# Optimization experiments

Hardware: AMD Instinct MI355X
Metric: run time of the kernel (lower is better)

## Reference

```python
import jax, jax.numpy as jnp
import numpy as np

N_NODES = 50000
N_EDGES = 800000
IN_CH = 64
OC = 16  # out_channels


def setup_inputs() -> dict:
    key = jax.random.key(0)
    ks = jax.random.split(key, 16)
    x = jax.random.normal(ks[0], (N_NODES, IN_CH), dtype=jnp.float32)
    edge_index = jax.random.randint(ks[1], (2, N_EDGES), 0, N_NODES, dtype=jnp.int64)

    def lin(k, fan_in, fan_out):
        s = 1.0 / np.sqrt(fan_in)
        return jax.random.uniform(k, (fan_in, fan_out), jnp.float32, -s, s)

    d1, d2 = 16 * OC, 8 * OC  # 256, 128
    return {
        "x": x,
        "W1_rel": lin(ks[2], IN_CH, d1), "b1": jnp.zeros((d1,), jnp.float32), "W1_root": lin(ks[3], IN_CH, d1),
        "W2_rel": lin(ks[4], d1, d2), "b2": jnp.zeros((d2,), jnp.float32), "W2_root": lin(ks[5], d1, d2),
        "Wmu_rel": lin(ks[6], d2, OC), "bmu": jnp.zeros((OC,), jnp.float32), "Wmu_root": lin(ks[7], d2, OC),
        "Wls_rel": lin(ks[8], d2, OC), "bls": jnp.zeros((OC,), jnp.float32), "Wls_root": lin(ks[9], d2, OC),
        "edge_index": edge_index,
    }


def _graph_conv(x, src, dst, deg_inv, W_rel, b, W_root):
    # PyG GraphConv(aggr='mean'): out = lin_rel(mean_{j in N(i)} x_j) + lin_root(x_i)
    msg_sum = jax.ops.segment_sum(x[src], dst, num_segments=x.shape[0])  # [N, d]
    agg = msg_sum * deg_inv[:, None]
    return agg @ W_rel + b + x @ W_root


def reference(x, W1_rel, b1, W1_root, W2_rel, b2, W2_root,
              Wmu_rel, bmu, Wmu_root, Wls_rel, bls, Wls_root, edge_index):
    src, dst = edge_index[0], edge_index[1]
    deg = jax.ops.segment_sum(jnp.ones_like(dst, dtype=x.dtype), dst, num_segments=x.shape[0])
    deg_inv = jnp.where(deg > 0, 1.0 / jnp.maximum(deg, 1.0), 0.0)

    h = jax.nn.relu(_graph_conv(x, src, dst, deg_inv, W1_rel, b1, W1_root))
    h = jax.nn.relu(_graph_conv(h, src, dst, deg_inv, W2_rel, b2, W2_root))
    mu = _graph_conv(h, src, dst, deg_inv, Wmu_rel, bmu, Wmu_root)
    logstd = _graph_conv(h, src, dst, deg_inv, Wls_rel, bls, Wls_root)
    return (mu, logstd)
```

## Files before the change

### kernel.cpp

```cpp
#include <hip/hip_runtime.h>
#include <hip/hip_fp8.h>

#define N_NODES 50000
#define N_EDGES 800000
#define NBUCK 196
#define PBLK 391
#define CAP 5120

typedef unsigned short ushort_t;
typedef unsigned char uchar_t;
typedef short short8 __attribute__((ext_vector_type(8)));
typedef short short4v __attribute__((ext_vector_type(4)));
typedef float floatx4 __attribute__((ext_vector_type(4)));
typedef float floatx2 __attribute__((ext_vector_type(2)));

__device__ __forceinline__ float bf2f(ushort_t u) {
    unsigned v = ((unsigned)u) << 16;
    return __builtin_bit_cast(float, v);
}
__device__ __forceinline__ ushort_t f2bf(float f) {
    unsigned u = __builtin_bit_cast(unsigned, f);
    unsigned r = (u + 0x7FFFu + ((u >> 16) & 1u)) >> 16;
    return (ushort_t)r;
}
__device__ __forceinline__ uchar_t f2fp8(float f) {
    return (uchar_t)(__builtin_amdgcn_cvt_pk_fp8_f32(f, f, 0, false) & 0xFF);
}
__device__ __forceinline__ float4 ld4(const float* p) { return *(const float4*)p; }

__device__ __forceinline__ void lite_barrier() {
    asm volatile("s_waitcnt lgkmcnt(0)" ::: "memory");
    __builtin_amdgcn_s_barrier();
}

__device__ __forceinline__ void acc16(float* a, uint4 v) {
    unsigned ws[4] = {v.x, v.y, v.z, v.w};
    #pragma unroll
    for (int wi = 0; wi < 4; ++wi) {
        floatx2 lo = __builtin_amdgcn_cvt_pk_f32_fp8(ws[wi], false);
        floatx2 hi = __builtin_amdgcn_cvt_pk_f32_fp8(ws[wi], true);
        a[wi * 4 + 0] += lo.x; a[wi * 4 + 1] += lo.y;
        a[wi * 4 + 2] += hi.x; a[wi * 4 + 3] += hi.y;
    }
}
__device__ __forceinline__ void acc8(float* a, uint2 v) {
    floatx2 p0 = __builtin_amdgcn_cvt_pk_f32_fp8(v.x, false);
    floatx2 p1 = __builtin_amdgcn_cvt_pk_f32_fp8(v.x, true);
    floatx2 p2 = __builtin_amdgcn_cvt_pk_f32_fp8(v.y, false);
    floatx2 p3 = __builtin_amdgcn_cvt_pk_f32_fp8(v.y, true);
    a[0] += p0.x; a[1] += p0.y; a[2] += p1.x; a[3] += p1.y;
    a[4] += p2.x; a[5] += p2.y; a[6] += p3.x; a[7] += p3.y;
}

__global__ __launch_bounds__(256) void prep_kernel(
    const float* __restrict__ x,
    const float* __restrict__ W1_rel, const float* __restrict__ W1_root,
    const float* __restrict__ W2_rel, const float* __restrict__ W2_root,
    const float* __restrict__ Wmu_rel, const float* __restrict__ Wls_rel,
    const float* __restrict__ Wmu_root, const float* __restrict__ Wls_root,
    ushort_t* __restrict__ xb, uchar_t* __restrict__ xq,
    ushort_t* __restrict__ B1t, ushort_t* __restrict__ B2t, ushort_t* __restrict__ B3t,
    int* __restrict__ bcursor) {
    int idx = blockIdx.x * blockDim.x + threadIdx.x;
    if (idx < 400000) {
        int n = idx >> 3, c = (idx & 7) * 8;
        float4 v0 = ld4(x + (size_t)n * 64 + c);
        float4 v1 = ld4(x + (size_t)n * 64 + c + 4);
        float vv[8] = {v0.x, v0.y, v0.z, v0.w, v1.x, v1.y, v1.z, v1.w};
        short8 o;
        #pragma unroll
        for (int i = 0; i < 8; ++i) o[i] = f2bf(vv[i]);
        int q0 = __builtin_amdgcn_cvt_pk_fp8_f32(vv[0], vv[1], 0, false);
        q0 = __builtin_amdgcn_cvt_pk_fp8_f32(vv[2], vv[3], q0, true);
        int q1 = __builtin_amdgcn_cvt_pk_fp8_f32(vv[4], vv[5], 0, false);
        q1 = __builtin_amdgcn_cvt_pk_fp8_f32(vv[6], vv[7], q1, true);
        *(short8*)(xb + (size_t)n * 64 + c) = o;
        uint2 q = {(unsigned)q0, (unsigned)q1};
        *(uint2*)(xq + (size_t)n * 64 + c) = q;
    } else if (idx < 506496) {
        int j = idx - 400000;
        if (j < 32768) {
            int n = j >> 7, k = j & 127;
            float v = (k < 64) ? W1_rel[k * 256 + n] : W1_root[(k - 64) * 256 + n];
            B1t[j] = f2bf(v);
        } else if (j < 98304) {
            int jj = j - 32768;
            int n = jj >> 8, k = jj & 255;
            float v = (n < 128) ? W2_rel[k * 128 + n] : W2_root[k * 128 + (n - 128)];
            B2t[jj] = f2bf(v);
        } else {
            int jj = j - 98304;
            int n = jj >> 7, k = jj & 127;
            const float* W = (n < 16) ? Wmu_rel : (n < 32) ? Wls_rel : (n < 48) ? Wmu_root : Wls_root;
            B3t[jj] = f2bf(W[k * 16 + (n & 15)]);
        }
    } else if (idx < 506496 + NBUCK) {
        int b = idx - 506496;
        bcursor[b] = b * CAP;
    }
}

__global__ __launch_bounds__(512) void partition_kernel(
    const int* __restrict__ src, const int* __restrict__ dst,
    int* __restrict__ bcursor, unsigned* __restrict__ pairbuf) {
    __shared__ int h[NBUCK];
    __shared__ int cur[NBUCK];
    const int tid = threadIdx.x;
    for (int i = tid; i < NBUCK; i += 512) h[i] = 0;
    __syncthreads();
    const int base = blockIdx.x * 2048;
    int d[4];
    #pragma unroll
    for (int j = 0; j < 4; ++j) {
        int e = base + j * 512 + tid;
        if (e < N_EDGES) { d[j] = dst[e]; atomicAdd(&h[d[j] >> 8], 1); }
        else d[j] = -1;
    }
    __syncthreads();
    for (int i = tid; i < NBUCK; i += 512) {
        int c = h[i];
        cur[i] = c ? atomicAdd(&bcursor[i], c) : 0;
    }
    __syncthreads();
    #pragma unroll
    for (int j = 0; j < 4; ++j) {
        int e = base + j * 512 + tid;
        if (e < N_EDGES) {
            int dd = d[j];
            int slot = atomicAdd(&cur[dd >> 8], 1);
            pairbuf[slot] = (unsigned)src[e] | ((unsigned)(dd & 255) << 16);
        }
    }
}

__global__ __launch_bounds__(1024) void fill_bucket_kernel(
    const unsigned* __restrict__ pairbuf, const int* __restrict__ bcursor,
    int* __restrict__ row_beg, int* __restrict__ row_end,
    float* __restrict__ dinv, ushort_t* __restrict__ eidx) {
    __shared__ int h[256];
    __shared__ int sm[256];
    __shared__ int cur[256];
    const int b = blockIdx.x, tid = threadIdx.x;
    const int beg = b * CAP, end = bcursor[b];
    if (tid < 256) h[tid] = 0;
    __syncthreads();
    for (int i = beg + tid; i < end; i += 1024)
        atomicAdd(&h[pairbuf[i] >> 16], 1);
    __syncthreads();
    if (tid < 256) sm[tid] = h[tid];
    __syncthreads();
    #pragma unroll
    for (int off = 1; off < 256; off <<= 1) {
        int t = 0;
        if (tid < 256 && tid >= off) t = sm[tid - off];
        __syncthreads();
        if (tid < 256) sm[tid] += t;
        __syncthreads();
    }
    if (tid < 256) {
        int c = h[tid];
        int exc = beg + sm[tid] - c;
        int node = b * 256 + tid;
        if (node < N_NODES) {
            row_beg[node] = exc;
            row_end[node] = exc + c;
            dinv[node] = c > 0 ? 1.0f / (float)c : 0.0f;
        }
        cur[tid] = exc;
    }
    __syncthreads();
    for (int i = beg + tid; i < end; i += 1024) {
        unsigned v = pairbuf[i];
        int slot = atomicAdd(&cur[v >> 16], 1);
        eidx[slot] = (ushort_t)(v & 0xFFFFu);
    }
}

__global__ __launch_bounds__(256) void g1gemm12(
    const ushort_t* __restrict__ xb, const uchar_t* __restrict__ xq,
    const int* __restrict__ row_beg, const int* __restrict__ row_end,
    const ushort_t* __restrict__ eidx, const float* __restrict__ dinv,
    const ushort_t* __restrict__ B1t, const float* __restrict__ b1,
    const ushort_t* __restrict__ B2t, ushort_t* __restrict__ h1g,
    uchar_t* __restrict__ t2, ushort_t* __restrict__ r2) {
    constexpr int K1 = 128, K2 = 256;
    constexpr int AKP = 72;
    constexpr int BKP = 136;
    __shared__ ushort_t Bs[64 * BKP];
    ushort_t* As = Bs;
    const int tid = threadIdx.x;
    const int rowbase = blockIdx.x * 64;

    {
        const int nl = tid >> 2, lane = tid & 3;
        const int node = rowbase + nl;
        int beg = 0, end = 0;
        float d = 0.0f;
        if (node < N_NODES) { beg = row_beg[node]; end = row_end[node]; d = dinv[node]; }
        float a0[16] = {}, a1[16] = {};
        int j = beg;
        for (; j + 3 < end; j += 4) {
            uint4 v0 = *(const uint4*)(xq + (size_t)eidx[j] * 64 + lane * 16);
            uint4 v1 = *(const uint4*)(xq + (size_t)eidx[j + 1] * 64 + lane * 16);
            uint4 v2 = *(const uint4*)(xq + (size_t)eidx[j + 2] * 64 + lane * 16);
            uint4 v3 = *(const uint4*)(xq + (size_t)eidx[j + 3] * 64 + lane * 16);
            acc16(a0, v0); acc16(a1, v1); acc16(a0, v2); acc16(a1, v3);
        }
        for (; j < end; ++j) {
            uint4 v0 = *(const uint4*)(xq + (size_t)eidx[j] * 64 + lane * 16);
            acc16(a0, v0);
        }
        short8 o0, o1;
        #pragma unroll
        for (int i = 0; i < 8; ++i) {
            o0[i] = f2bf((a0[i] + a1[i]) * d);
            o1[i] = f2bf((a0[8 + i] + a1[8 + i]) * d);
        }
        *(short8*)(As + nl * AKP + lane * 16) = o0;
        *(short8*)(As + nl * AKP + lane * 16 + 8) = o1;
    }
    __syncthreads();

    const int w = tid >> 6, lane64 = tid & 63;
    const int ln = lane64 & 15, quad = lane64 >> 4;
    const int rwl = w * 16 + ln;
    int r = rowbase + rwl;
    if (r > N_NODES - 1) r = N_NODES - 1;

    float bias[4][4];
    #pragma unroll
    for (int ny = 0; ny < 4; ++ny)
        #pragma unroll
        for (int f = 0; f < 4; ++f)
            bias[ny][f] = b1[ny * 64 + f * 16 + ln];

    short8 a[4];
    a[0] = *(const short8*)(As + rwl * AKP + quad * 8);
    a[1] = *(const short8*)(As + rwl * AKP + 32 + quad * 8);
    a[2] = *(const short8*)(xb + (size_t)r * 64 + quad * 8);
    a[3] = *(const short8*)(xb + (size_t)r * 64 + 32 + quad * 8);
    short8 pb[4];
    #pragma unroll
    for (int i = 0; i < 4; ++i) {
        int idx = tid + i * 256, row = idx >> 4, off = (idx & 15) * 8;
        pb[i] = *(const short8*)(B1t + (size_t)row * K1 + off);
    }
    for (int ny = 0; ny < 4; ++ny) {
        lite_barrier();
        #pragma unroll
        for (int i = 0; i < 4; ++i) {
            int idx = tid + i * 256, row = idx >> 4, off = (idx & 15) * 8;
            *(short8*)(Bs + row * BKP + off) = pb[i];
        }
        if (ny < 3) {
            #pragma unroll
            for (int i = 0; i < 4; ++i) {
                int idx = tid + i * 256, row = idx >> 4, off = (idx & 15) * 8;
                pb[i] = *(const short8*)(B1t + (size_t)((ny + 1) * 64 + row) * K1 + off);
            }
        } else {
            #pragma unroll
            for (int i = 0; i < 4; ++i) {
                int idx = tid + i * 256, row = idx >> 4, off = (idx & 15) * 8;
                pb[i] = *(const short8*)(B2t + (size_t)row * K2 + off);
            }
        }
        lite_barrier();
        floatx4 acc[4] = {};
        #pragma unroll
        for (int f = 0; f < 4; ++f) {
            const ushort_t* bp = Bs + (f * 16 + ln) * BKP + quad * 8;
            #pragma unroll
            for (int s = 0; s < 4; ++s) {
                short8 b = *(const short8*)(bp + s * 32);
                acc[f] = __builtin_amdgcn_mfma_f32_16x16x32_bf16(a[s], b, acc[f], 0, 0, 0);
            }
        }
        lite_barrier();
        #pragma unroll
        for (int f = 0; f < 4; ++f) {
            int nl0 = f * 16 + ln;
            #pragma unroll
            for (int g = 0; g < 4; ++g) {
                int rr = w * 16 + quad * 4 + g;
                Bs[rr * AKP + nl0] = f2bf(fmaxf(acc[f][g] + bias[ny][f], 0.0f));
            }
        }
        lite_barrier();
        {
            int row2 = tid >> 2, seg = tid & 3;
            int gr = rowbase + row2;
            if (gr < N_NODES) {
                const uint4* s4 = (const uint4*)(Bs + row2 * AKP + seg * 16);
                uint4* d4 = (uint4*)(h1g + (size_t)gr * 256 + ny * 64 + seg * 16);
                d4[0] = s4[0]; d4[1] = s4[1];
            }
        }
    }
    __syncthreads();

    short8 a2[8];
    #pragma unroll
    for (int s = 0; s < 8; ++s)
        a2[s] = *(const short8*)(h1g + (size_t)r * 256 + s * 32 + quad * 8);
    for (int ny = 0; ny < 4; ++ny) {
        floatx4 acc[4] = {};
        #pragma unroll
        for (int kh = 0; kh < 2; ++kh) {
            lite_barrier();
            #pragma unroll
            for (int i = 0; i < 4; ++i) {
                int idx = tid + i * 256, row = idx >> 4, off = (idx & 15) * 8;
                *(short8*)(Bs + row * BKP + off) = pb[i];
            }
            int st = ny * 2 + kh;
            if (st < 7) {
                int nyn = (st + 1) >> 1, khn = (st + 1) & 1;
                #pragma unroll
                for (int i = 0; i < 4; ++i) {
                    int idx = tid + i * 256, row = idx >> 4, off = (idx & 15) * 8;
                    pb[i] = *(const short8*)(B2t + (size_t)(nyn * 64 + row) * K2 + khn * 128 + off);
                }
            }
            lite_barrier();
            #pragma unroll
            for (int f = 0; f < 4; ++f) {
                const ushort_t* bp = Bs + (f * 16 + ln) * BKP + quad * 8;
                #pragma unroll
                for (int s = 0; s < 4; ++s) {
                    short8 b = *(const short8*)(bp + s * 32);
                    acc[f] = __builtin_amdgcn_mfma_f32_16x16x32_bf16(a2[kh * 4 + s], b, acc[f], 0, 0, 0);
                }
            }
        }
        lite_barrier();
        if (ny < 2) {
            uchar_t* Ob = (uchar_t*)Bs;
            #pragma unroll
            for (int f = 0; f < 4; ++f) {
                int nl0 = f * 16 + ln;
                #pragma unroll
                for (int g = 0; g < 4; ++g) {
                    int rr = w * 16 + quad * 4 + g;
                    Ob[rr * 80 + nl0] = f2fp8(acc[f][g]);
                }
            }
            lite_barrier();
            int row2 = tid >> 2, seg = tid & 3;
            int gr = rowbase + row2;
            if (gr < N_NODES)
                *(uint4*)(t2 + (size_t)gr * 128 + ny * 64 + seg * 16) =
                    *(const uint4*)(Ob + row2 * 80 + seg * 16);
        } else {
            #pragma unroll
            for (int f = 0; f < 4; ++f) {
                int nl0 = f * 16 + ln;
                #pragma unroll
                for (int g = 0; g < 4; ++g) {
                    int rr = w * 16 + quad * 4 + g;
                    Bs[rr * AKP + nl0] = f2bf(acc[f][g]);
                }
            }
            lite_barrier();
            int row2 = tid >> 2, seg = tid & 3;
            int gr = rowbase + row2;
            if (gr < N_NODES) {
                const uint4* s4 = (const uint4*)(Bs + row2 * AKP + seg * 16);
                uint4* d4 = (uint4*)(r2 + (size_t)gr * 128 + (ny - 2) * 64 + seg * 16);
                d4[0] = s4[0]; d4[1] = s4[1];
            }
        }
    }
}

__global__ __launch_bounds__(256) void g2g3_kernel(
    const uchar_t* __restrict__ t2, const ushort_t* __restrict__ r2,
    const int* __restrict__ row_beg, const int* __restrict__ row_end,
    const ushort_t* __restrict__ eidx, const float* __restrict__ dinv,
    const float* __restrict__ b2, const ushort_t* __restrict__ B3t,
    ushort_t* __restrict__ tml, float* __restrict__ rml) {
    constexpr int KP = 136;
    __shared__ ushort_t As[16 * KP];
    const int tid = threadIdx.x;
    const int nb = blockIdx.x * 16;
    {
        const int nl = tid >> 4, lane = tid & 15;
        const int node = nb + nl;
        const int beg = row_beg[node], end = row_end[node];
        float a0[8] = {}, a1[8] = {}, a2[8] = {}, a3[8] = {};
        int j = beg;
        for (; j + 3 < end; j += 4) {
            uint2 v0 = *(const uint2*)(t2 + (size_t)eidx[j] * 128 + lane * 8);
            uint2 v1 = *(const uint2*)(t2 + (size_t)eidx[j + 1] * 128 + lane * 8);
            uint2 v2 = *(const uint2*)(t2 + (size_t)eidx[j + 2] * 128 + lane * 8);
            uint2 v3 = *(const uint2*)(t2 + (size_t)eidx[j + 3] * 128 + lane * 8);
            acc8(a0, v0); acc8(a1, v1); acc8(a2, v2); acc8(a3, v3);
        }
        for (; j < end; ++j) {
            uint2 v0 = *(const uint2*)(t2 + (size_t)eidx[j] * 128 + lane * 8);
            acc8(a0, v0);
        }
        float d = dinv[node];
        short8 rv = *(const short8*)(r2 + (size_t)node * 128 + lane * 8);
        float4 ba = ld4(b2 + lane * 8), bb = ld4(b2 + lane * 8 + 4);
        float bc[8] = {ba.x, ba.y, ba.z, ba.w, bb.x, bb.y, bb.z, bb.w};
        short8 o;
        #pragma unroll
        for (int i = 0; i < 8; ++i)
            o[i] = f2bf(fmaxf(((a0[i] + a1[i]) + (a2[i] + a3[i])) * d + bf2f((ushort_t)rv[i]) + bc[i], 0.0f));
        *(short8*)(As + nl * KP + lane * 8) = o;
    }
    __syncthreads();
    const int w = tid >> 6, lane64 = tid & 63;
    const int ln = lane64 & 15, quad = lane64 >> 4;
    short8 a[4];
    #pragma unroll
    for (int s = 0; s < 4; ++s)
        a[s] = *(const short8*)(As + ln * KP + s * 32 + quad * 8);
    floatx4 acc = {};
    const ushort_t* bp = B3t + (size_t)(w * 16 + ln) * 128 + quad * 8;
    #pragma unroll
    for (int s = 0; s < 4; ++s) {
        short8 b = *(const short8*)(bp + s * 32);
        acc = __builtin_amdgcn_mfma_f32_16x16x32_bf16(a[s], b, acc, 0, 0, 0);
    }
    const int r0 = nb + quad * 4;
    const int ncol = w * 16 + ln;
    #pragma unroll
    for (int g = 0; g < 4; ++g) {
        int rr = r0 + g;
        float v = acc[g];
        if (ncol < 32) tml[(size_t)rr * 32 + ncol] = f2bf(v);
        else rml[(size_t)rr * 32 + (ncol - 32)] = v;
    }
}

__global__ __launch_bounds__(256) void gather3_kernel(
    const ushort_t* __restrict__ tml, const float* __restrict__ rml,
    const int* __restrict__ row_beg, const int* __restrict__ row_end,
    const ushort_t* __restrict__ eidx, const float* __restrict__ dinv,
    const float* __restrict__ bmu, const float* __restrict__ bls,
    float* __restrict__ out) {
    const int lane = threadIdx.x & 7;
    const int nl = threadIdx.x >> 3;
    const int n = blockIdx.x * 32 + nl;
    if (n >= N_NODES) return;
    const int beg = row_beg[n], end = row_end[n];
    float a0[4] = {}, a1[4] = {}, a2[4] = {}, a3[4] = {};
    int j = beg;
    for (; j + 3 < end; j += 4) {
        short4v v0 = *(const short4v*)(tml + (size_t)eidx[j] * 32 + lane * 4);
        short4v v1 = *(const short4v*)(tml + (size_t)eidx[j + 1] * 32 + lane * 4);
        short4v v2 = *(const short4v*)(tml + (size_t)eidx[j + 2] * 32 + lane * 4);
        short4v v3 = *(const short4v*)(tml + (size_t)eidx[j + 3] * 32 + lane * 4);
        #pragma unroll
        for (int i = 0; i < 4; ++i) {
            a0[i] += bf2f((ushort_t)v0[i]); a1[i] += bf2f((ushort_t)v1[i]);
            a2[i] += bf2f((ushort_t)v2[i]); a3[i] += bf2f((ushort_t)v3[i]);
        }
    }
    for (; j < end; ++j) {
        short4v v0 = *(const short4v*)(tml + (size_t)eidx[j] * 32 + lane * 4);
        #pragma unroll
        for (int i = 0; i < 4; ++i) a0[i] += bf2f((ushort_t)v0[i]);
    }
    float d = dinv[n];
    const float* bias = (lane < 4) ? (bmu + lane * 4) : (bls + (lane - 4) * 4);
    float4 ra = ld4(rml + (size_t)n * 32 + lane * 4);
    float4 ba = ld4(bias);
    float rr[4] = {ra.x, ra.y, ra.z, ra.w};
    float bc[4] = {ba.x, ba.y, ba.z, ba.w};
    float res[4];
    #pragma unroll
    for (int i = 0; i < 4; ++i) res[i] = ((a0[i] + a1[i]) + (a2[i] + a3[i])) * d + rr[i] + bc[i];
    float* base = (lane < 4) ? (out + (size_t)n * 16 + lane * 4)
                             : (out + 800000u + (size_t)n * 16 + (lane - 4) * 4);
    *(float4*)(base) = make_float4(res[0], res[1], res[2], res[3]);
}

extern "C" void kernel_launch(void* const* d_in, const int* in_sizes, int n_in,
                              void* d_out, int out_size, void* d_ws, size_t ws_size,
                              hipStream_t stream) {
    const float* x       = (const float*)d_in[0];
    const float* W1_rel  = (const float*)d_in[1];
    const float* b1      = (const float*)d_in[2];
    const float* W1_root = (const float*)d_in[3];
    const float* W2_rel  = (const float*)d_in[4];
    const float* b2      = (const float*)d_in[5];
    const float* W2_root = (const float*)d_in[6];
    const float* Wmu_rel = (const float*)d_in[7];
    const float* bmu     = (const float*)d_in[8];
    const float* Wmu_root= (const float*)d_in[9];
    const float* Wls_rel = (const float*)d_in[10];
    const float* bls     = (const float*)d_in[11];
    const float* Wls_root= (const float*)d_in[12];
    const int*   ei      = (const int*)d_in[13];
    const int* src = ei;
    const int* dst = ei + N_EDGES;

    int*      bcursor = (int*)d_ws;
    int*      row_beg = bcursor + 256;
    int*      row_end = row_beg + 50048;
    unsigned* pairbuf = (unsigned*)(row_end + 50048);
    ushort_t* eidx    = (ushort_t*)(pairbuf + 1003520);
    float*    dinv    = (float*)(eidx + 1003520);
    ushort_t* xb   = (ushort_t*)(dinv + 50000);
    uchar_t*  xq   = (uchar_t*)(xb + 3200000);
    uchar_t*  t2   = xq + 3200000;
    ushort_t* r2   = (ushort_t*)(t2 + 6400000);
    ushort_t* tml  = r2 + 6400000;
    ushort_t* B1t  = tml + 1600000;
    ushort_t* B2t  = B1t + 32768;
    ushort_t* B3t  = B2t + 65536;
    float* rml     = (float*)(B3t + 8192);
    ushort_t* h1g  = (ushort_t*)(rml + 1600000);
    float* out     = (float*)d_out;

    prep_kernel<<<1980, 256, 0, stream>>>(x, W1_rel, W1_root, W2_rel, W2_root,
                                          Wmu_rel, Wls_rel, Wmu_root, Wls_root,
                                          xb, xq, B1t, B2t, B3t, bcursor);
    partition_kernel<<<PBLK, 512, 0, stream>>>(src, dst, bcursor, pairbuf);
    fill_bucket_kernel<<<NBUCK, 1024, 0, stream>>>(pairbuf, bcursor, row_beg, row_end, dinv, eidx);

    g1gemm12<<<782, 256, 0, stream>>>(xb, xq, row_beg, row_end, eidx, dinv,
                                      B1t, b1, B2t, h1g, t2, r2);

    g2g3_kernel<<<3125, 256, 0, stream>>>(t2, r2, row_beg, row_end, eidx, dinv, b2, B3t, tml, rml);

    gather3_kernel<<<1563, 256, 0, stream>>>(tml, rml, row_beg, row_end, eidx, dinv, bmu, bls, out);
}
```

Before: 192.7 us.

## Double-buffer weight tiles in LDS and swizzle epilogue stores in fused GEMM kernel

Measured after the change: 191.2 us (median of 2 runs). About the same (-0.8%).

```diff
diff --git a/kernel.cpp b/kernel.cpp
--- a/kernel.cpp
+++ b/kernel.cpp
@@ -186,8 +186,8 @@
     constexpr int K1 = 128, K2 = 256;
     constexpr int AKP = 72;
     constexpr int BKP = 136;
-    __shared__ ushort_t Bs[64 * BKP];
-    ushort_t* As = Bs;
+    __shared__ ushort_t Bs[2][64 * BKP];
+    ushort_t* As = Bs[0];
     const int tid = threadIdx.x;
     const int rowbase = blockIdx.x * 64;
 
@@ -239,37 +239,38 @@
     a[1] = *(const short8*)(As + rwl * AKP + 32 + quad * 8);
     a[2] = *(const short8*)(xb + (size_t)r * 64 + quad * 8);
     a[3] = *(const short8*)(xb + (size_t)r * 64 + 32 + quad * 8);
+
+    const int sb_row = tid >> 4;
+    const int sb_off = (tid & 15) * 8;
+    #define STRIP_SRC(u, i) ((u) < 4 \
+        ? (const short8*)(B1t + (size_t)((u) * 64 + sb_row + (i) * 16) * K1 + sb_off) \
+        : (const short8*)(B2t + (size_t)((((u) - 4) >> 1) * 64 + sb_row + (i) * 16) * K2 + (((u) - 4) & 1) * 128 + sb_off))
+
     short8 pb[4];
     #pragma unroll
-    for (int i = 0; i < 4; ++i) {
-        int idx = tid + i * 256, row = idx >> 4, off = (idx & 15) * 8;
-        pb[i] = *(const short8*)(B1t + (size_t)row * K1 + off);
-    }
+    for (int i = 0; i < 4; ++i) pb[i] = *STRIP_SRC(0, i);
+    #pragma unroll
+    for (int i = 0; i < 4; ++i)
+        *(short8*)(&Bs[1][(sb_row + i * 16) * BKP + sb_off]) = pb[i];
+    #pragma unroll
+    for (int i = 0; i < 4; ++i) pb[i] = *STRIP_SRC(1, i);
+    lite_barrier();
+    int cur = 1;
+
     for (int ny = 0; ny < 4; ++ny) {
         lite_barrier();
         #pragma unroll
-        for (int i = 0; i < 4; ++i) {
-            int idx = tid + i * 256, row = idx >> 4, off = (idx & 15) * 8;
-            *(short8*)(Bs + row * BKP + off) = pb[i];
-        }
-        if (ny < 3) {
+        for (int i = 0; i < 4; ++i)
+            *(short8*)(&Bs[cur ^ 1][(sb_row + i * 16) * BKP + sb_off]) = pb[i];
+        {
+            int u = ny + 2;
             #pragma unroll
-            for (int i = 0; i < 4; ++i) {
-                int idx = tid + i * 256, row = idx >> 4, off = (idx & 15) * 8;
-                pb[i] = *(const short8*)(B1t + (size_t)((ny + 1) * 64 + row) * K1 + off);
-            }
-        } else {
-            #pragma unroll
-            for (int i = 0; i < 4; ++i) {
-                int idx = tid + i * 256, row = idx >> 4, off = (idx & 15) * 8;
-                pb[i] = *(const short8*)(B2t + (size_t)row * K2 + off);
-            }
-        }
-        lite_barrier();
+            for (int i = 0; i < 4; ++i) pb[i] = *STRIP_SRC(u, i);
+        }
         floatx4 acc[4] = {};
         #pragma unroll
         for (int f = 0; f < 4; ++f) {
-            const ushort_t* bp = Bs + (f * 16 + ln) * BKP + quad * 8;
+            const ushort_t* bp = &Bs[cur][(f * 16 + ln) * BKP + quad * 8];
             #pragma unroll
             for (int s = 0; s < 4; ++s) {
                 short8 b = *(const short8*)(bp + s * 32);
@@ -279,23 +280,24 @@
         lite_barrier();
         #pragma unroll
         for (int f = 0; f < 4; ++f) {
-            int nl0 = f * 16 + ln;
+            int nl0 = (f * 16 + ln) ^ (quad << 4);
             #pragma unroll
             for (int g = 0; g < 4; ++g) {
                 int rr = w * 16 + quad * 4 + g;
-                Bs[rr * AKP + nl0] = f2bf(fmaxf(acc[f][g] + bias[ny][f], 0.0f));
+                Bs[cur][rr * AKP + nl0] = f2bf(fmaxf(acc[f][g] + bias[ny][f], 0.0f));
             }
         }
         lite_barrier();
         {
-            int row2 = tid >> 2, seg = tid & 3;
+            int row2 = tid >> 2, seg = tid & 3, q2 = (row2 >> 2) & 3;
             int gr = rowbase + row2;
             if (gr < N_NODES) {
-                const uint4* s4 = (const uint4*)(Bs + row2 * AKP + seg * 16);
+                const uint4* s4 = (const uint4*)(&Bs[cur][row2 * AKP + ((seg ^ q2) << 4)]);
                 uint4* d4 = (uint4*)(h1g + (size_t)gr * 256 + ny * 64 + seg * 16);
                 d4[0] = s4[0]; d4[1] = s4[1];
             }
         }
+        cur ^= 1;
     }
     __syncthreads();
 
@@ -303,42 +305,39 @@
     #pragma unroll
     for (int s = 0; s < 8; ++s)
         a2[s] = *(const short8*)(h1g + (size_t)r * 256 + s * 32 + quad * 8);
-    for (int ny = 0; ny < 4; ++ny) {
+    for (int ny2 = 0; ny2 < 4; ++ny2) {
         floatx4 acc[4] = {};
         #pragma unroll
         for (int kh = 0; kh < 2; ++kh) {
+            int st = 4 + ny2 * 2 + kh;
             lite_barrier();
-            #pragma unroll
-            for (int i = 0; i < 4; ++i) {
-                int idx = tid + i * 256, row = idx >> 4, off = (idx & 15) * 8;
-                *(short8*)(Bs + row * BKP + off) = pb[i];
-            }
-            int st = ny * 2 + kh;
-            if (st < 7) {
-                int nyn = (st + 1) >> 1, khn = (st + 1) & 1;
+            if (st < 11) {
                 #pragma unroll
-                for (int i = 0; i < 4; ++i) {
-                    int idx = tid + i * 256, row = idx >> 4, off = (idx & 15) * 8;
-                    pb[i] = *(const short8*)(B2t + (size_t)(nyn * 64 + row) * K2 + khn * 128 + off);
+                for (int i = 0; i < 4; ++i)
+                    *(short8*)(&Bs[cur ^ 1][(sb_row + i * 16) * BKP + sb_off]) = pb[i];
+                if (st < 10) {
+                    int u = st + 2;
+                    #pragma unroll
+                    for (int i = 0; i < 4; ++i) pb[i] = *STRIP_SRC(u, i);
                 }
             }
-            lite_barrier();
             #pragma unroll
             for (int f = 0; f < 4; ++f) {
-                const ushort_t* bp = Bs + (f * 16 + ln) * BKP + quad * 8;
+                const ushort_t* bp = &Bs[cur][(f * 16 + ln) * BKP + quad * 8];
                 #pragma unroll
                 for (int s = 0; s < 4; ++s) {
                     short8 b = *(const short8*)(bp + s * 32);
                     acc[f] = __builtin_amdgcn_mfma_f32_16x16x32_bf16(a2[kh * 4 + s], b, acc[f], 0, 0, 0);
                 }
             }
+            if (kh == 0) cur ^= 1;
         }
         lite_barrier();
-        if (ny < 2) {
-            uchar_t* Ob = (uchar_t*)Bs;
+        if (ny2 < 2) {
+            uchar_t* Ob = (uchar_t*)Bs[cur];
             #pragma unroll
             for (int f = 0; f < 4; ++f) {
-                int nl0 = f * 16 + ln;
+                int nl0 = (f * 16 + ln) ^ (quad << 4);
                 #pragma unroll
                 for (int g = 0; g < 4; ++g) {
                     int rr = w * 16 + quad * 4 + g;
@@ -346,31 +345,33 @@
                 }
             }
             lite_barrier();
-            int row2 = tid >> 2, seg = tid & 3;
+            int row2 = tid >> 2, seg = tid & 3, q2 = (row2 >> 2) & 3;
             int gr = rowbase + row2;
             if (gr < N_NODES)
-                *(uint4*)(t2 + (size_t)gr * 128 + ny * 64 + seg * 16) =
-                    *(const uint4*)(Ob + row2 * 80 + seg * 16);
+                *(uint4*)(t2 + (size_t)gr * 128 + ny2 * 64 + seg * 16) =
+                    *(const uint4*)(Ob + row2 * 80 + ((seg ^ q2) << 4));
         } else {
             #pragma unroll
             for (int f = 0; f < 4; ++f) {
-                int nl0 = f * 16 + ln;
+                int nl0 = (f * 16 + ln) ^ (quad << 4);
                 #pragma unroll
                 for (int g = 0; g < 4; ++g) {
                     int rr = w * 16 + quad * 4 + g;
-                    Bs[rr * AKP + nl0] = f2bf(acc[f][g]);
+                    Bs[cur][rr * AKP + nl0] = f2bf(acc[f][g]);
                 }
             }
             lite_barrier();
-            int row2 = tid >> 2, seg = tid & 3;
+            int row2 = tid >> 2, seg = tid & 3, q2 = (row2 >> 2) & 3;
             int gr = rowbase + row2;
             if (gr < N_NODES) {
-                const uint4* s4 = (const uint4*)(Bs + row2 * AKP + seg * 16);
-                uint4* d4 = (uint4*)(r2 + (size_t)gr * 128 + (ny - 2) * 64 + seg * 16);
+                const uint4* s4 = (const uint4*)(&Bs[cur][row2 * AKP + ((seg ^ q2) << 4)]);
+                uint4* d4 = (uint4*)(r2 + (size_t)gr * 128 + (ny2 - 2) * 64 + seg * 16);
                 d4[0] = s4[0]; d4[1] = s4[1];
             }
         }
-    }
+        cur ^= 1;
+    }
+    #undef STRIP_SRC
 }
 
 __global__ __launch_bounds__(256) void g2g3_kernel(
```
